# Kernel tuning notes

Measured on AMD Instinct MI355X. Metric: run time of the kernel, lower is better.

Reference implementation:

```python
import jax, jax.numpy as jnp
import numpy as np

T = 200                      # TRAIN_ROIS_PER_IMAGE
RATIO = 0.33                 # ROI_POSITIVE_RATIO
P_MAX = int(T * RATIO)       # max positive ROIs (66)
MH, MW = 28, 28              # MASK_SHAPE
STD = jnp.array([0.1, 0.1, 0.2, 0.2], jnp.float32)  # BBOX_STD_DEV
EPS = 1e-6


def _iou(a, b):
    # a [N,4], b [G,4] -> [N,G] IoU (same math as overlaps_graph, without tiling)
    ay1, ax1, ay2, ax2 = a[:, 0:1], a[:, 1:2], a[:, 2:3], a[:, 3:4]
    by1, bx1, by2, bx2 = b[None, :, 0], b[None, :, 1], b[None, :, 2], b[None, :, 3]
    iy = jnp.maximum(jnp.minimum(ay2, by2) - jnp.maximum(ay1, by1), 0.0)
    ix = jnp.maximum(jnp.minimum(ax2, bx2) - jnp.maximum(ax1, bx1), 0.0)
    inter = iy * ix
    union = (ay2 - ay1) * (ax2 - ax1) + (by2 - by1) * (bx2 - bx1) - inter
    return inter / jnp.maximum(union, EPS)


def _box_refinement(box, gt):
    # standard Mask R-CNN box_refinement_graph
    h = jnp.maximum(box[:, 2] - box[:, 0], EPS)
    w = jnp.maximum(box[:, 3] - box[:, 1], EPS)
    cy = box[:, 0] + 0.5 * h
    cx = box[:, 1] + 0.5 * w
    gh = jnp.maximum(gt[:, 2] - gt[:, 0], EPS)
    gw = jnp.maximum(gt[:, 3] - gt[:, 1], EPS)
    gcy = gt[:, 0] + 0.5 * gh
    gcx = gt[:, 1] + 0.5 * gw
    return jnp.stack([(gcy - cy) / h, (gcx - cx) / w,
                      jnp.log(gh / h), jnp.log(gw / w)], axis=-1)


def _crop_and_resize(imgs, boxes):
    # imgs [T,H,W], boxes [T,4] normalized; TF crop_and_resize bilinear semantics,
    # extrapolation_value = 0 for samples outside [0, H-1] x [0, W-1].
    Tn, H, W = imgs.shape
    y1, x1, y2, x2 = boxes[:, 0], boxes[:, 1], boxes[:, 2], boxes[:, 3]
    iy = jnp.arange(MH, dtype=jnp.float32)
    ix = jnp.arange(MW, dtype=jnp.float32)
    ys = y1[:, None] * (H - 1) + iy[None, :] * ((y2 - y1) * (H - 1) / (MH - 1))[:, None]  # [T,MH]
    xs = x1[:, None] * (W - 1) + ix[None, :] * ((x2 - x1) * (W - 1) / (MW - 1))[:, None]  # [T,MW]
    y0 = jnp.floor(ys); x0 = jnp.floor(xs)
    wy = (ys - y0)[:, :, None]
    wx = (xs - x0)[:, None, :]
    y0i = jnp.clip(y0, 0, H - 1).astype(jnp.int32)
    y1i = jnp.clip(y0 + 1, 0, H - 1).astype(jnp.int32)
    x0i = jnp.clip(x0, 0, W - 1).astype(jnp.int32)
    x1i = jnp.clip(x0 + 1, 0, W - 1).astype(jnp.int32)
    t = jnp.arange(Tn)[:, None, None]
    v00 = imgs[t, y0i[:, :, None], x0i[:, None, :]]
    v01 = imgs[t, y0i[:, :, None], x1i[:, None, :]]
    v10 = imgs[t, y1i[:, :, None], x0i[:, None, :]]
    v11 = imgs[t, y1i[:, :, None], x1i[:, None, :]]
    val = (v00 * (1 - wx) + v01 * wx) * (1 - wy) + (v10 * (1 - wx) + v11 * wx) * wy
    ok = ((ys >= 0) & (ys <= H - 1))[:, :, None] & ((xs >= 0) & (xs <= W - 1))[:, None, :]
    return jnp.where(ok, val, 0.0)


def _targets_one(proposals, class_ids, boxes, masks):
    # proposals [N,4], class_ids [G] int, boxes [G,4], masks [H,W,G]
    N = proposals.shape[0]
    # zero-padding trim expressed as validity masks (jit-friendly fixed shapes)
    valid_prop = jnp.any(proposals != 0, axis=1)
    valid_gt = jnp.any(boxes != 0, axis=1)
    non_crowd = (class_ids > 0) & valid_gt
    crowd = (class_ids < 0) & valid_gt

    ov = _iou(proposals, boxes)                              # [N,G]
    ov_nc = jnp.where(non_crowd[None, :], ov, -1.0)          # mask crowd/padded gt
    roi_iou_max = ov_nc.max(axis=1)
    crowd_max = jnp.where(crowd[None, :], ov, 0.0).max(axis=1)

    pos_mask = valid_prop & (roi_iou_max >= 0.5)
    neg_mask = valid_prop & (roi_iou_max < 0.5) & (crowd_max < 0.001)

    # deterministic selection (original uses tf.random.shuffle): positives first-in-order
    pos_order = jnp.argsort(jnp.where(pos_mask, 0, 1))
    neg_order = jnp.argsort(jnp.where(neg_mask, 0, 1))
    pos_count = jnp.minimum(pos_mask.sum(), P_MAX)
    neg_needed = jnp.floor(pos_count.astype(jnp.float32) / RATIO).astype(jnp.int32) - pos_count
    neg_count = jnp.minimum(jnp.minimum(neg_needed, neg_mask.sum()), T - pos_count)

    slot = jnp.arange(T)
    is_pos = slot < pos_count
    is_neg = (slot >= pos_count) & (slot < pos_count + neg_count)
    src = jnp.where(is_pos,
                    pos_order[jnp.clip(slot, 0, N - 1)],
                    neg_order[jnp.clip(slot - pos_count, 0, N - 1)])
    rois = jnp.where((is_pos | is_neg)[:, None], proposals[src], 0.0)

    assign = jnp.argmax(ov_nc[src], axis=1)                  # gt assignment per slot
    gt_box = boxes[assign]
    gt_cls = jnp.where(is_pos, class_ids[assign], 0)

    deltas = _box_refinement(rois, gt_box) / STD
    deltas = jnp.where(is_pos[:, None], deltas, 0.0)

    # USE_MINI_MASK: roi box in gt-box-normalized coordinates
    gy1, gx1, gy2, gx2 = gt_box[:, 0], gt_box[:, 1], gt_box[:, 2], gt_box[:, 3]
    gh = jnp.maximum(gy2 - gy1, EPS)
    gw = jnp.maximum(gx2 - gx1, EPS)
    mm = jnp.stack([(rois[:, 0] - gy1) / gh, (rois[:, 1] - gx1) / gw,
                    (rois[:, 2] - gy1) / gh, (rois[:, 3] - gx1) / gw], axis=-1)

    roi_masks = jnp.moveaxis(jnp.take(masks, assign, axis=2), 2, 0)  # [T,H,W]
    m = jnp.round(_crop_and_resize(roi_masks, mm))
    m = jnp.where(is_pos[:, None, None], m, 0.0)
    return rois, gt_cls, deltas, m


def setup_inputs() -> dict:
    key = jax.random.key(0)
    ks = jax.random.split(key, 4)
    B, N, G, HM = 16, 2000, 200, 56

    def boxes_of(k, shape):
        k1, k2, k3, k4 = jax.random.split(k, 4)
        y1 = jax.random.uniform(k1, shape) * 0.5
        x1 = jax.random.uniform(k2, shape) * 0.5
        h = 0.1 + jax.random.uniform(k3, shape) * 0.4
        w = 0.1 + jax.random.uniform(k4, shape) * 0.4
        return jnp.stack([y1, x1, y1 + h, x1 + w], axis=-1)

    proposals = boxes_of(ks[0], (B, N))
    proposals = proposals * (jnp.arange(N) < N - 200)[None, :, None]  # zero-padded tail
    prior_class_ids = jax.random.randint(ks[1], (B, G), -1, 81).astype(jnp.int32)  # -1=crowd, 0=padding
    prior_boxes = boxes_of(ks[2], (B, G)) * (prior_class_ids != 0)[..., None]
    prior_masks = (jax.random.uniform(ks[3], (B, HM, HM, G)) > 0.5).astype(jnp.float32)
    return {"proposals": proposals, "prior_class_ids": prior_class_ids,
            "prior_boxes": prior_boxes, "prior_masks": prior_masks}


def reference(proposals, prior_class_ids, prior_boxes, prior_masks):
    rois, cls, deltas, masks = jax.vmap(_targets_one)(proposals, prior_class_ids,
                                                      prior_boxes, prior_masks)
    return rois, cls, deltas, masks
```

## Files before the change

### kernel.cpp

```cpp
#include <hip/hip_runtime.h>
#include <math.h>

#pragma clang fp contract(off)

#define BN    16
#define NP    2000
#define NG    200
#define NT    200
#define PMAX  66
#define EPSF  1e-6f
#define MH    28
#define MW    28
#define HM    56
#define NPIX  (HM*HM)
#define NSLOT 128
#define NW    49

__global__ __launch_bounds__(256) void kA(
    const float* __restrict__ proposals, const int* __restrict__ cls_ids,
    const float* __restrict__ boxes,
    int* __restrict__ flag_ws, int* __restrict__ assign_ws)
{
#pragma clang fp contract(off)
  const int b = blockIdx.y;
  __shared__ float4 gbox[NG];
  __shared__ float  garea[NG];
  __shared__ int    gflag[NG];

  for (int j = threadIdx.x; j < NG; j += 256) {
    float4 g = reinterpret_cast<const float4*>(boxes + (size_t)b * NG * 4)[j];
    int c = cls_ids[b * NG + j];
    bool vg = (g.x != 0.f) || (g.y != 0.f) || (g.z != 0.f) || (g.w != 0.f);
    gbox[j]  = g;
    garea[j] = (g.z - g.x) * (g.w - g.y);
    gflag[j] = vg ? (c > 0 ? 1 : (c < 0 ? 2 : 0)) : 0;
  }
  __syncthreads();

  int i = blockIdx.x * 256 + threadIdx.x;
  if (i >= NP) return;

  float4 p = reinterpret_cast<const float4*>(proposals + (size_t)b * NP * 4)[i];
  bool vp = (p.x != 0.f) || (p.y != 0.f) || (p.z != 0.f) || (p.w != 0.f);
  float pa = (p.z - p.x) * (p.w - p.y);

  float best = -3.0e38f;
  int   bestj = 0;
  float cmax = 0.f;
  for (int j = 0; j < NG; ++j) {
    float4 g = gbox[j];
    float iy = fmaxf(fminf(p.z, g.z) - fmaxf(p.x, g.x), 0.f);
    float ix = fmaxf(fminf(p.w, g.w) - fmaxf(p.y, g.y), 0.f);
    float inter = iy * ix;
    float uni = (pa + garea[j]) - inter;
    float iou = inter / fmaxf(uni, EPSF);
    int fl = gflag[j];
    float v = (fl == 1) ? iou : -1.0f;
    if (v > best) { best = v; bestj = j; }
    if (fl == 2) cmax = fmaxf(cmax, iou);
  }
  bool pos = vp && (best >= 0.5f);
  bool neg = vp && (best < 0.5f) && (cmax < 0.001f);
  flag_ws[b * NP + i]   = pos ? 1 : (neg ? 2 : 0);
  assign_ws[b * NP + i] = bestj;
}

__global__ __launch_bounds__(256) void kB(
    const float* __restrict__ proposals, const int* __restrict__ cls_ids,
    const float* __restrict__ boxes, const int* __restrict__ flag_ws,
    const int* __restrict__ assign_ws, float* __restrict__ out,
    float* __restrict__ mm_ws, int* __restrict__ ma_ws)
{
#pragma clang fp contract(off)
  const int b = blockIdx.x;
  const int tid = threadIdx.x;
  const int lane = tid & 63;
  const int wv = tid >> 6;

  __shared__ unsigned short pos_list[NP];
  __shared__ unsigned short neg_list[NP];
  __shared__ int wcp[4], wcn[4];
  __shared__ int s_pt, s_nt;
  if (tid == 0) { s_pt = 0; s_nt = 0; }
  __syncthreads();

  const int* fb = flag_ws + b * NP;
  for (int base = 0; base < NP; base += 256) {
    int i = base + tid;
    int f = (i < NP) ? fb[i] : 0;
    bool isp = (f == 1), isn = (f == 2);
    unsigned long long bp = __ballot(isp);
    unsigned long long bn = __ballot(isn);
    __syncthreads();
    if (lane == 0) { wcp[wv] = __popcll(bp); wcn[wv] = __popcll(bn); }
    __syncthreads();
    int prep = __popcll(bp & ((1ull << lane) - 1ull));
    int pren = __popcll(bn & ((1ull << lane) - 1ull));
    int bpp = 0, bnn = 0, tp = 0, tn = 0;
    for (int w = 0; w < 4; ++w) {
      if (w < wv) { bpp += wcp[w]; bnn += wcn[w]; }
      tp += wcp[w]; tn += wcn[w];
    }
    int pt = s_pt, nt = s_nt;
    if (isp) pos_list[pt + bpp + prep] = (unsigned short)i;
    if (isn) neg_list[nt + bnn + pren] = (unsigned short)i;
    __syncthreads();
    if (tid == 0) { s_pt = pt + tp; s_nt = nt + tn; }
  }
  __syncthreads();

  int pos_total = s_pt, neg_total = s_nt;
  int pos_count = min(pos_total, PMAX);
  int neg_needed = (int)floorf((float)pos_count / 0.33f) - pos_count;
  int neg_count = min(min(neg_needed, neg_total), NT - pos_count);

  if (tid < NT) {
    bool ispos = tid < pos_count;
    bool isneg = (!ispos) && (tid < pos_count + neg_count);
    float r0 = 0.f, r1 = 0.f, r2 = 0.f, r3 = 0.f;
    float d0 = 0.f, d1 = 0.f, d2 = 0.f, d3 = 0.f;
    float m0 = 0.f, m1 = 0.f, m2 = 0.f, m3 = 0.f;
    float clsf = 0.f;
    int ma = -1;
    if (ispos || isneg) {
      int i = ispos ? (int)pos_list[tid] : (int)neg_list[tid - pos_count];
      float4 p = reinterpret_cast<const float4*>(proposals + (size_t)b * NP * 4)[i];
      r0 = p.x; r1 = p.y; r2 = p.z; r3 = p.w;
      if (ispos) {
        int a = assign_ws[b * NP + i];
        ma = a;
        float4 g = reinterpret_cast<const float4*>(boxes + (size_t)b * NG * 4)[a];
        float h  = fmaxf(r2 - r0, EPSF);
        float w  = fmaxf(r3 - r1, EPSF);
        float cy = r0 + 0.5f * h;
        float cx = r1 + 0.5f * w;
        float gh = fmaxf(g.z - g.x, EPSF);
        float gw = fmaxf(g.w - g.y, EPSF);
        float gcy = g.x + 0.5f * gh;
        float gcx = g.y + 0.5f * gw;
        d0 = ((gcy - cy) / h) / 0.1f;
        d1 = ((gcx - cx) / w) / 0.1f;
        d2 = logf(gh / h) / 0.2f;
        d3 = logf(gw / w) / 0.2f;
        m0 = (r0 - g.x) / gh;
        m1 = (r1 - g.y) / gw;
        m2 = (r2 - g.x) / gh;
        m3 = (r3 - g.y) / gw;
        clsf = (float)cls_ids[b * NG + a];
      }
    }
    int s = b * NT + tid;
    float* rois = out;
    float* cls  = out + BN * NT * 4;
    float* dlt  = out + BN * NT * 4 + BN * NT;
    rois[s * 4 + 0] = r0; rois[s * 4 + 1] = r1;
    rois[s * 4 + 2] = r2; rois[s * 4 + 3] = r3;
    cls[s] = clsf;
    dlt[s * 4 + 0] = d0; dlt[s * 4 + 1] = d1;
    dlt[s * 4 + 2] = d2; dlt[s * 4 + 3] = d3;
    mm_ws[s * 4 + 0] = m0; mm_ws[s * 4 + 1] = m1;
    mm_ws[s * 4 + 2] = m2; mm_ws[s * 4 + 3] = m3;
    ma_ws[s] = ma;
  }
}

__global__ __launch_bounds__(256) void kG(
    const float* __restrict__ masks, const int* __restrict__ ma_ws,
    unsigned long long* __restrict__ bits)
{
  const int b  = blockIdx.z;
  const int s0 = blockIdx.y * 64;
  const int p0 = blockIdx.x * 64;
  __shared__ unsigned long long sw[64];
  __shared__ int sma[64];
  const int tid  = threadIdx.x;
  const int lane = tid & 63;
  const int wv   = tid >> 6;
  if (tid < 64) sma[tid] = ma_ws[b * NT + s0 + tid];
  __syncthreads();

  const int g = sma[lane];
  const float* mbase = masks + (size_t)b * NPIX * NG;
  for (int e = 0; e < 16; ++e) {
    int pl = e * 4 + wv;
    float v = 0.f;
    if (g >= 0) v = mbase[(size_t)(p0 + pl) * NG + g];
    unsigned long long word = __ballot(v != 0.f);
    if (lane == 0) sw[pl] = word;
  }
  __syncthreads();

  unsigned long long w0 = sw[lane];
  for (int k = 0; k < 16; ++k) {
    int sl = wv * 16 + k;
    unsigned long long word = __ballot((int)((w0 >> sl) & 1ULL));
    if (lane == 0 && sma[sl] >= 0)
      bits[(size_t)(b * NSLOT + s0 + sl) * NW + blockIdx.x] = word;
  }
}

__global__ __launch_bounds__(256) void kC(
    const unsigned long long* __restrict__ bits, const float* __restrict__ mm_ws,
    const int* __restrict__ ma_ws, float* __restrict__ out)
{
#pragma clang fp contract(off)
  const int s = blockIdx.x;
  float4* om = reinterpret_cast<float4*>(
      out + (size_t)(BN * NT * 9) + (size_t)s * (MH * MW));
  const int q = threadIdx.x;
  const int a = ma_ws[s];
  if (a < 0) {
    if (q < (MH * MW) / 4) om[q] = make_float4(0.f, 0.f, 0.f, 0.f);
    return;
  }

  __shared__ unsigned long long pb[NW];
  const int b = s / NT;
  const int t = s - b * NT;
  if (q < NW) pb[q] = bits[(size_t)(b * NSLOT + t) * NW + q];
  __syncthreads();
  if (q >= (MH * MW) / 4) return;

  float y1 = mm_ws[s * 4 + 0], x1 = mm_ws[s * 4 + 1];
  float y2 = mm_ws[s * 4 + 2], x2 = mm_ws[s * 4 + 3];
  float sy = (y2 - y1) * 55.0f / 27.0f;
  float sx = (x2 - x1) * 55.0f / 27.0f;

  int px0 = q * 4;
  int my  = px0 / MW;
  float ys = y1 * 55.0f + (float)my * sy;
  float y0f = floorf(ys);
  float wy  = ys - y0f;
  int y0i = (int)fminf(fmaxf(y0f, 0.f), 55.f);
  int y1i = (int)fminf(fmaxf(y0f + 1.0f, 0.f), 55.f);
  bool oky = (ys >= 0.f) && (ys <= 55.f);
  const int r0b = y0i * HM;
  const int r1b = y1i * HM;

  float res[4];
  for (int k = 0; k < 4; ++k) {
    int mx = (px0 + k) - my * MW;
    float xs = x1 * 55.0f + (float)mx * sx;
    float x0f = floorf(xs);
    float wx  = xs - x0f;
    int x0i = (int)fminf(fmaxf(x0f, 0.f), 55.f);
    int x1i = (int)fminf(fmaxf(x0f + 1.0f, 0.f), 55.f);
    int p00 = r0b + x0i, p01 = r0b + x1i;
    int p10 = r1b + x0i, p11 = r1b + x1i;
    float v00 = (float)((pb[p00 >> 6] >> (p00 & 63)) & 1ULL);
    float v01 = (float)((pb[p01 >> 6] >> (p01 & 63)) & 1ULL);
    float v10 = (float)((pb[p10 >> 6] >> (p10 & 63)) & 1ULL);
    float v11 = (float)((pb[p11 >> 6] >> (p11 & 63)) & 1ULL);
    float val = (v00 * (1.f - wx) + v01 * wx) * (1.f - wy)
              + (v10 * (1.f - wx) + v11 * wx) * wy;
    bool ok = oky && (xs >= 0.f) && (xs <= 55.f);
    res[k] = ok ? rintf(val) : 0.f;
  }
  om[q] = make_float4(res[0], res[1], res[2], res[3]);
}

extern "C" void kernel_launch(void* const* d_in, const int* in_sizes, int n_in,
                              void* d_out, int out_size, void* d_ws, size_t ws_size,
                              hipStream_t stream)
{
  const float* proposals = (const float*)d_in[0];
  const int*   cls_ids   = (const int*)d_in[1];
  const float* boxes     = (const float*)d_in[2];
  const float* masks     = (const float*)d_in[3];
  float* out = (float*)d_out;

  char* ws = (char*)d_ws;
  int*   flag_ws   = (int*)ws;    ws += (size_t)BN * NP * sizeof(int);
  int*   assign_ws = (int*)ws;    ws += (size_t)BN * NP * sizeof(int);
  float* mm_ws     = (float*)ws;  ws += (size_t)BN * NT * 4 * sizeof(float);
  int*   ma_ws     = (int*)ws;    ws += (size_t)BN * NT * sizeof(int);
  unsigned long long* bits_ws = (unsigned long long*)ws;

  dim3 gA((NP + 255) / 256, BN);
  kA<<<gA, 256, 0, stream>>>(proposals, cls_ids, boxes, flag_ws, assign_ws);
  kB<<<BN, 256, 0, stream>>>(proposals, cls_ids, boxes, flag_ws, assign_ws,
                             out, mm_ws, ma_ws);
  dim3 gG(NPIX / 64, NSLOT / 64, BN);
  kG<<<gG, 256, 0, stream>>>(masks, ma_ws, bits_ws);
  kC<<<BN * NT, 256, 0, stream>>>(bits_ws, mm_ws, ma_ws, out);
}
```

Before: 126.9 us.

## Bitpack masks per GT box and fuse into IoU kernel launch

Mask bit-packing now runs per ground-truth box rather than per sampled ROI slot, which removes its dependency on kB's assignment output. It is merged into the same launch as the IoU/assignment kernel, so the two run concurrently and one launch is dropped. kC then looks up each ROI's bits by its assigned GT index. The cost is packing all 200 GT masks per image instead of only the sampled slots, which adds some memory reads.

```diff
diff --git a/kernel.cpp b/kernel.cpp
--- a/kernel.cpp
+++ b/kernel.cpp
@@ -13,56 +13,95 @@
 #define MW    28
 #define HM    56
 #define NPIX  (HM*HM)
-#define NSLOT 128
 #define NW    49
-
-__global__ __launch_bounds__(256) void kA(
+#define NGP   256
+
+#define KA_BLOCKS 128
+#define KG_BLOCKS (49*4*BN)
+
+__global__ __launch_bounds__(256) void kF(
     const float* __restrict__ proposals, const int* __restrict__ cls_ids,
-    const float* __restrict__ boxes,
-    int* __restrict__ flag_ws, int* __restrict__ assign_ws)
-{
-#pragma clang fp contract(off)
-  const int b = blockIdx.y;
+    const float* __restrict__ boxes, const float* __restrict__ masks,
+    int* __restrict__ flag_ws, int* __restrict__ assign_ws,
+    unsigned long long* __restrict__ bits)
+{
+#pragma clang fp contract(off)
+  const int tid  = threadIdx.x;
+  const int lane = tid & 63;
+  const int wv   = tid >> 6;
+
   __shared__ float4 gbox[NG];
   __shared__ float  garea[NG];
   __shared__ int    gflag[NG];
-
-  for (int j = threadIdx.x; j < NG; j += 256) {
-    float4 g = reinterpret_cast<const float4*>(boxes + (size_t)b * NG * 4)[j];
-    int c = cls_ids[b * NG + j];
-    bool vg = (g.x != 0.f) || (g.y != 0.f) || (g.z != 0.f) || (g.w != 0.f);
-    gbox[j]  = g;
-    garea[j] = (g.z - g.x) * (g.w - g.y);
-    gflag[j] = vg ? (c > 0 ? 1 : (c < 0 ? 2 : 0)) : 0;
-  }
-  __syncthreads();
-
-  int i = blockIdx.x * 256 + threadIdx.x;
-  if (i >= NP) return;
-
-  float4 p = reinterpret_cast<const float4*>(proposals + (size_t)b * NP * 4)[i];
-  bool vp = (p.x != 0.f) || (p.y != 0.f) || (p.z != 0.f) || (p.w != 0.f);
-  float pa = (p.z - p.x) * (p.w - p.y);
-
-  float best = -3.0e38f;
-  int   bestj = 0;
-  float cmax = 0.f;
-  for (int j = 0; j < NG; ++j) {
-    float4 g = gbox[j];
-    float iy = fmaxf(fminf(p.z, g.z) - fmaxf(p.x, g.x), 0.f);
-    float ix = fmaxf(fminf(p.w, g.w) - fmaxf(p.y, g.y), 0.f);
-    float inter = iy * ix;
-    float uni = (pa + garea[j]) - inter;
-    float iou = inter / fmaxf(uni, EPSF);
-    int fl = gflag[j];
-    float v = (fl == 1) ? iou : -1.0f;
-    if (v > best) { best = v; bestj = j; }
-    if (fl == 2) cmax = fmaxf(cmax, iou);
-  }
-  bool pos = vp && (best >= 0.5f);
-  bool neg = vp && (best < 0.5f) && (cmax < 0.001f);
-  flag_ws[b * NP + i]   = pos ? 1 : (neg ? 2 : 0);
-  assign_ws[b * NP + i] = bestj;
+  __shared__ unsigned long long sw[64];
+
+  if (blockIdx.x < KA_BLOCKS) {
+    const int b = blockIdx.x >> 3;
+    const int bxa = blockIdx.x & 7;
+
+    for (int j = tid; j < NG; j += 256) {
+      float4 g = reinterpret_cast<const float4*>(boxes + (size_t)b * NG * 4)[j];
+      int c = cls_ids[b * NG + j];
+      bool vg = (g.x != 0.f) || (g.y != 0.f) || (g.z != 0.f) || (g.w != 0.f);
+      gbox[j]  = g;
+      garea[j] = (g.z - g.x) * (g.w - g.y);
+      gflag[j] = vg ? (c > 0 ? 1 : (c < 0 ? 2 : 0)) : 0;
+    }
+    __syncthreads();
+
+    int i = bxa * 256 + tid;
+    if (i >= NP) return;
+
+    float4 p = reinterpret_cast<const float4*>(proposals + (size_t)b * NP * 4)[i];
+    bool vp = (p.x != 0.f) || (p.y != 0.f) || (p.z != 0.f) || (p.w != 0.f);
+    float pa = (p.z - p.x) * (p.w - p.y);
+
+    float best = -3.0e38f;
+    int   bestj = 0;
+    float cmax = 0.f;
+    for (int j = 0; j < NG; ++j) {
+      float4 g = gbox[j];
+      float iy = fmaxf(fminf(p.z, g.z) - fmaxf(p.x, g.x), 0.f);
+      float ix = fmaxf(fminf(p.w, g.w) - fmaxf(p.y, g.y), 0.f);
+      float inter = iy * ix;
+      float uni = (pa + garea[j]) - inter;
+      float iou = inter / fmaxf(uni, EPSF);
+      int fl = gflag[j];
+      float v = (fl == 1) ? iou : -1.0f;
+      if (v > best) { best = v; bestj = j; }
+      if (fl == 2) cmax = fmaxf(cmax, iou);
+    }
+    bool pos = vp && (best >= 0.5f);
+    bool neg = vp && (best < 0.5f) && (cmax < 0.001f);
+    flag_ws[b * NP + i]   = pos ? 1 : (neg ? 2 : 0);
+    assign_ws[b * NP + i] = bestj;
+  } else {
+    int idx = blockIdx.x - KA_BLOCKS;
+    const int pword = idx % 49;
+    idx /= 49;
+    const int gw0 = (idx & 3) * 64;
+    const int b   = idx >> 2;
+    const int p0  = pword * 64;
+
+    const bool gok = (gw0 + lane) < NG;
+    const float* mbase = masks + (size_t)b * NPIX * NG + gw0 + lane;
+    for (int e = 0; e < 16; ++e) {
+      int pl = e * 4 + wv;
+      float v = 0.f;
+      if (gok) v = mbase[(size_t)(p0 + pl) * NG];
+      unsigned long long word = __ballot(v != 0.f);
+      if (lane == 0) sw[pl] = word;
+    }
+    __syncthreads();
+
+    unsigned long long w0 = sw[lane];
+    for (int k = 0; k < 16; ++k) {
+      int gl = wv * 16 + k;
+      unsigned long long word = __ballot((int)((w0 >> gl) & 1ULL));
+      if (lane == 0 && (gw0 + gl) < NG)
+        bits[(size_t)(b * NGP + gw0 + gl) * NW + pword] = word;
+    }
+  }
 }
 
 __global__ __launch_bounds__(256) void kB(
@@ -164,41 +203,6 @@
   }
 }
 
-__global__ __launch_bounds__(256) void kG(
-    const float* __restrict__ masks, const int* __restrict__ ma_ws,
-    unsigned long long* __restrict__ bits)
-{
-  const int b  = blockIdx.z;
-  const int s0 = blockIdx.y * 64;
-  const int p0 = blockIdx.x * 64;
-  __shared__ unsigned long long sw[64];
-  __shared__ int sma[64];
-  const int tid  = threadIdx.x;
-  const int lane = tid & 63;
-  const int wv   = tid >> 6;
-  if (tid < 64) sma[tid] = ma_ws[b * NT + s0 + tid];
-  __syncthreads();
-
-  const int g = sma[lane];
-  const float* mbase = masks + (size_t)b * NPIX * NG;
-  for (int e = 0; e < 16; ++e) {
-    int pl = e * 4 + wv;
-    float v = 0.f;
-    if (g >= 0) v = mbase[(size_t)(p0 + pl) * NG + g];
-    unsigned long long word = __ballot(v != 0.f);
-    if (lane == 0) sw[pl] = word;
-  }
-  __syncthreads();
-
-  unsigned long long w0 = sw[lane];
-  for (int k = 0; k < 16; ++k) {
-    int sl = wv * 16 + k;
-    unsigned long long word = __ballot((int)((w0 >> sl) & 1ULL));
-    if (lane == 0 && sma[sl] >= 0)
-      bits[(size_t)(b * NSLOT + s0 + sl) * NW + blockIdx.x] = word;
-  }
-}
-
 __global__ __launch_bounds__(256) void kC(
     const unsigned long long* __restrict__ bits, const float* __restrict__ mm_ws,
     const int* __restrict__ ma_ws, float* __restrict__ out)
@@ -216,8 +220,7 @@
 
   __shared__ unsigned long long pb[NW];
   const int b = s / NT;
-  const int t = s - b * NT;
-  if (q < NW) pb[q] = bits[(size_t)(b * NSLOT + t) * NW + q];
+  if (q < NW) pb[q] = bits[(size_t)(b * NGP + a) * NW + q];
   __syncthreads();
   if (q >= (MH * MW) / 4) return;
 
@@ -276,11 +279,9 @@
   int*   ma_ws     = (int*)ws;    ws += (size_t)BN * NT * sizeof(int);
   unsigned long long* bits_ws = (unsigned long long*)ws;
 
-  dim3 gA((NP + 255) / 256, BN);
-  kA<<<gA, 256, 0, stream>>>(proposals, cls_ids, boxes, flag_ws, assign_ws);
+  kF<<<KA_BLOCKS + KG_BLOCKS, 256, 0, stream>>>(
+      proposals, cls_ids, boxes, masks, flag_ws, assign_ws, bits_ws);
   kB<<<BN, 256, 0, stream>>>(proposals, cls_ids, boxes, flag_ws, assign_ws,
                              out, mm_ws, ma_ws);
-  dim3 gG(NPIX / 64, NSLOT / 64, BN);
-  kG<<<gG, 256, 0, stream>>>(masks, ma_ws, bits_ws);
   kC<<<BN * NT, 256, 0, stream>>>(bits_ws, mm_ws, ma_ws, out);
 }
```

New measurement: 112.3 us. 1.13x faster.
